# Kernel tuning notes

Measured on AMD Instinct MI355X. Metric: run time of the kernel, lower is better.

Reference implementation:

```python
import jax, jax.numpy as jnp
import numpy as np

B, C, T = 16, 2048, 128      # batch, enc_in (variables), d_model
ID, NC, CD, GD, OUT = 32, 16, 32, 32, 96  # id_dim, num_clusters, cluster_dim, graph_dim, out_len
GIN = T + ID + CD            # gcn_input_dim = 192
NEG = -1.0e9


def setup_inputs() -> dict:
    key = jax.random.key(0)
    ks = jax.random.split(key, 13)
    s = 0.02
    return {
        "x": jax.random.normal(ks[0], (B, C, 1, T), dtype=jnp.float32),
        "id_emb": jax.random.normal(ks[1], (C, ID), dtype=jnp.float32) * s,
        "w1": jax.random.normal(ks[2], (T, T // 2), dtype=jnp.float32) * s,
        "b1": jnp.zeros((T // 2,), dtype=jnp.float32),
        "w2": jax.random.normal(ks[3], (T // 2, ID), dtype=jnp.float32) * s,
        "b2": jnp.zeros((ID,), dtype=jnp.float32),
        "cluster_emb": jax.random.normal(ks[4], (NC, CD), dtype=jnp.float32) * s,
        "wic": jax.random.normal(ks[5], (ID, CD), dtype=jnp.float32) * s,
        "bic": jnp.zeros((CD,), dtype=jnp.float32),
        "wg": jax.random.normal(ks[6], (ID + CD, GD), dtype=jnp.float32) * s,
        "bg": jnp.zeros((GD,), dtype=jnp.float32),
        "context_weight": jax.random.normal(ks[7], (C, GIN), dtype=jnp.float32) * s,
        "wl": jax.random.normal(ks[8], (GIN, OUT), dtype=jnp.float32) * s,
        "bl": jnp.zeros((OUT,), dtype=jnp.float32),
    }


def reference(x, id_emb, w1, b1, w2, b2, cluster_emb, wic, bic, wg, bg,
              context_weight, wl, bl):
    b, c, n, t = x.shape
    xs = x[:, :, 0, :]                                       # [b,c,t] (squeeze dim -2)
    # dynamic id projection: Linear -> ReLU -> Linear
    dyn = jax.nn.relu(xs @ w1 + b1) @ w2 + b2                # [b,c,id]
    id_embeds = id_emb[None, :, :] + dyn                     # static + dynamic
    # soft cluster assignment
    id_for_clustering = id_embeds @ wic + bic                # [b,c,cd]
    probs = jax.nn.softmax(
        jnp.einsum('bcl,nl->bcn', id_for_clustering, cluster_emb), axis=-1)
    cluster_embeds = probs @ cluster_emb                     # [b,c,cd]
    # graph embedding and dynamic dense adjacency
    graph_emb = jnp.concatenate([id_embeds, cluster_embeds], axis=-1) @ wg + bg
    adj = jnp.einsum('bcg,bmg->bcm', graph_emb, graph_emb)   # [b,c,c]
    adj = jax.nn.relu(adj)
    neg = NEG * jnp.eye(c, dtype=adj.dtype)                  # [c,c], -1e9 on diag, 0 off-diag
    adj = adj + neg
    # torch.where(adj<=0, neg_inf_matrix, adj): off-diag nonpositive -> 0, diag -> -1e9
    adj = jnp.where(adj <= 0.0, neg, adj)
    adj = jax.nn.softmax(adj, axis=-1)
    # two-stage GCN aggregation (dropout is identity in eval mode)
    gcn_input = jnp.concatenate([xs, id_embeds, cluster_embeds], axis=-1)  # [b,c,GIN]
    agg = jnp.einsum('boi,bid->bod', adj, gcn_input)         # [b,c,GIN]
    w = jnp.tanh(jnp.einsum('bod,ol->bdl', agg, context_weight))  # [b,GIN,GIN]
    out = (jnp.einsum('bdl,bod->bol', w, gcn_input) + gcn_input) @ wl + bl  # [b,c,out_len]
    return out[:, :, None, :]                                # unsqueeze dim -2
```

## Files before the change

### kernel.cpp

```cpp
#include <hip/hip_runtime.h>
#include <hip/hip_bf16.h>


typedef __attribute__((ext_vector_type(8))) short short8;
typedef __attribute__((ext_vector_type(16))) float f32x16;

__device__ __forceinline__ unsigned short f2bf(float f) {
    __hip_bfloat16 h = __float2bfloat16(f);
    return *reinterpret_cast<unsigned short*>(&h);
}
__device__ __forceinline__ float bf2f(unsigned short u) {
    __hip_bfloat16 h = *reinterpret_cast<__hip_bfloat16*>(&u);
    return __bfloat162float(h);
}

__global__ __launch_bounds__(256) void k0_transpose_x(
    const float* __restrict__ x, unsigned short* __restrict__ vt)
{
    __shared__ float sT[64 * 133];
    const int t = threadIdx.x;
    const int m0 = blockIdx.x * 64;
    const int b = blockIdx.y;
    const float* xb = x + (size_t)b * 2048 * 128;
    #pragma unroll
    for (int kk = 0; kk < 8; ++kk) {
        int i = t + kk * 256;
        int mm = i >> 5, q4 = i & 31;
        float4 v = ((const float4*)(xb + (size_t)(m0 + mm) * 128))[q4];
        float* d = sT + mm * 133 + q4 * 4;
        d[0] = v.x; d[1] = v.y; d[2] = v.z; d[3] = v.w;
    }
    __syncthreads();
    const int mp = t & 31;
    const int ch0 = t >> 5;
    #pragma unroll
    for (int pass = 0; pass < 16; ++pass) {
        int ch = ch0 + pass * 8;
        unsigned int u0 = f2bf(sT[(2 * mp) * 133 + ch]);
        unsigned int u1 = f2bf(sT[(2 * mp + 1) * 133 + ch]);
        *((unsigned int*)(vt + (size_t)(b * 192 + ch) * 2048 + m0) + mp) =
            u0 | (u1 << 16);
    }
}

__global__ __launch_bounds__(256) void k1_tiled(
    const float* __restrict__ x, const float* __restrict__ id_emb,
    const float* __restrict__ w1, const float* __restrict__ b1,
    const float* __restrict__ w2, const float* __restrict__ b2,
    const float* __restrict__ ce, const float* __restrict__ wic,
    const float* __restrict__ bic, const float* __restrict__ wg,
    const float* __restrict__ bg, unsigned short* __restrict__ vt,
    unsigned short* __restrict__ geb16)
{
    __shared__ float sh[32 * 68];
    __shared__ float sid[32 * 36];
    __shared__ float sic[32 * 36];
    __shared__ float scl[32 * 36];
    __shared__ float sp[32 * 20];

    const int t = threadIdx.x;
    const int r0 = blockIdx.x * 32;
    const int b = r0 >> 11;
    const int c0 = r0 & 2047;

    {
        const int row = t >> 3, j0 = (t & 7) * 8;
        const float* xrow = x + (size_t)(r0 + row) * 128;
        float acc[8];
        #pragma unroll
        for (int j = 0; j < 8; ++j) acc[j] = b1[j0 + j];
        float4 pa[4], pb[4];
        float4 pxv;
        #pragma unroll
        for (int u = 0; u < 4; ++u) {
            const float4* wr = (const float4*)(w1 + u * 64 + j0);
            pa[u] = wr[0]; pb[u] = wr[1];
        }
        pxv = *(const float4*)(xrow);
        for (int k0 = 0; k0 < 128; k0 += 4) {
            float4 ca[4], cb[4];
            float4 cxv = pxv;
            #pragma unroll
            for (int u = 0; u < 4; ++u) { ca[u] = pa[u]; cb[u] = pb[u]; }
            const int kn = k0 + 4;
            if (kn < 128) {
                #pragma unroll
                for (int u = 0; u < 4; ++u) {
                    const float4* wr = (const float4*)(w1 + (kn + u) * 64 + j0);
                    pa[u] = wr[0]; pb[u] = wr[1];
                }
                pxv = *(const float4*)(xrow + kn);
            }
            float cx[4] = {cxv.x, cxv.y, cxv.z, cxv.w};
            #pragma unroll
            for (int u = 0; u < 4; ++u) {
                acc[0] = fmaf(cx[u], ca[u].x, acc[0]);
                acc[1] = fmaf(cx[u], ca[u].y, acc[1]);
                acc[2] = fmaf(cx[u], ca[u].z, acc[2]);
                acc[3] = fmaf(cx[u], ca[u].w, acc[3]);
                acc[4] = fmaf(cx[u], cb[u].x, acc[4]);
                acc[5] = fmaf(cx[u], cb[u].y, acc[5]);
                acc[6] = fmaf(cx[u], cb[u].z, acc[6]);
                acc[7] = fmaf(cx[u], cb[u].w, acc[7]);
            }
        }
        float* hr = sh + row * 68 + j0;
        #pragma unroll
        for (int j = 0; j < 8; ++j) hr[j] = fmaxf(acc[j], 0.f);
    }
    __syncthreads();

    {
        const int row = t >> 3, j0 = (t & 7) * 4;
        const int c = c0 + row;
        const float* hrow = sh + row * 68;
        float acc[4];
        #pragma unroll
        for (int j = 0; j < 4; ++j) acc[j] = b2[j0 + j];
        float4 pw[4];
        float  ph[4];
        #pragma unroll
        for (int u = 0; u < 4; ++u) {
            pw[u] = *(const float4*)(w2 + u * 32 + j0);
            ph[u] = hrow[u];
        }
        for (int k0 = 0; k0 < 64; k0 += 4) {
            float4 cw4[4];
            float  ch4[4];
            #pragma unroll
            for (int u = 0; u < 4; ++u) { cw4[u] = pw[u]; ch4[u] = ph[u]; }
            const int kn = k0 + 4;
            if (kn < 64) {
                #pragma unroll
                for (int u = 0; u < 4; ++u) {
                    pw[u] = *(const float4*)(w2 + (kn + u) * 32 + j0);
                    ph[u] = hrow[kn + u];
                }
            }
            #pragma unroll
            for (int u = 0; u < 4; ++u) {
                acc[0] = fmaf(ch4[u], cw4[u].x, acc[0]);
                acc[1] = fmaf(ch4[u], cw4[u].y, acc[1]);
                acc[2] = fmaf(ch4[u], cw4[u].z, acc[2]);
                acc[3] = fmaf(ch4[u], cw4[u].w, acc[3]);
            }
        }
        #pragma unroll
        for (int j = 0; j < 4; ++j) {
            float ide = id_emb[c * 32 + j0 + j] + acc[j];
            sid[row * 36 + j0 + j] = ide;
            vt[(size_t)(b * 192 + 128 + j0 + j) * 2048 + c] = f2bf(ide);
        }
    }
    __syncthreads();

    {
        const int row = t >> 3, j0 = (t & 7) * 4;
        const float* irow = sid + row * 36;
        float acc[4];
        #pragma unroll
        for (int j = 0; j < 4; ++j) acc[j] = bic[j0 + j];
        float4 pw[4];
        float  pi[4];
        #pragma unroll
        for (int u = 0; u < 4; ++u) {
            pw[u] = *(const float4*)(wic + u * 32 + j0);
            pi[u] = irow[u];
        }
        for (int k0 = 0; k0 < 32; k0 += 4) {
            float4 cw4[4];
            float  ci4[4];
            #pragma unroll
            for (int u = 0; u < 4; ++u) { cw4[u] = pw[u]; ci4[u] = pi[u]; }
            const int kn = k0 + 4;
            if (kn < 32) {
                #pragma unroll
                for (int u = 0; u < 4; ++u) {
                    pw[u] = *(const float4*)(wic + (kn + u) * 32 + j0);
                    pi[u] = irow[kn + u];
                }
            }
            #pragma unroll
            for (int u = 0; u < 4; ++u) {
                acc[0] = fmaf(ci4[u], cw4[u].x, acc[0]);
                acc[1] = fmaf(ci4[u], cw4[u].y, acc[1]);
                acc[2] = fmaf(ci4[u], cw4[u].z, acc[2]);
                acc[3] = fmaf(ci4[u], cw4[u].w, acc[3]);
            }
        }
        #pragma unroll
        for (int j = 0; j < 4; ++j) sic[row * 36 + j0 + j] = acc[j];
    }
    __syncthreads();

    {
        const int n = t & 15, rowp = t >> 4;
        const float* cer = ce + n * 32;
        float a0 = 0.f, a1 = 0.f;
        #pragma unroll
        for (int k0 = 0; k0 < 32; k0 += 8) {
            float cv[8], s0[8], s1[8];
            #pragma unroll
            for (int u = 0; u < 8; ++u) {
                cv[u] = cer[k0 + u];
                s0[u] = sic[rowp * 36 + k0 + u];
                s1[u] = sic[(rowp + 16) * 36 + k0 + u];
            }
            #pragma unroll
            for (int u = 0; u < 8; ++u) {
                a0 = fmaf(s0[u], cv[u], a0);
                a1 = fmaf(s1[u], cv[u], a1);
            }
        }
        sp[rowp * 20 + n] = a0;
        sp[(rowp + 16) * 20 + n] = a1;
    }
    __syncthreads();

    if (t < 32) {
        float* pr = sp + t * 20;
        float mx = pr[0];
        for (int n = 1; n < 16; ++n) mx = fmaxf(mx, pr[n]);
        float ss = 0.f;
        for (int n = 0; n < 16; ++n) { float e = __expf(pr[n] - mx); pr[n] = e; ss += e; }
        float inv = 1.f / ss;
        for (int n = 0; n < 16; ++n) pr[n] *= inv;
    }
    __syncthreads();

    {
        const int row = t >> 3, j0 = (t & 7) * 4;
        const int c = c0 + row;
        const float* prow = sp + row * 20;
        float acc[4] = {0.f, 0.f, 0.f, 0.f};
        float4 pc[4];
        float  pp[4];
        #pragma unroll
        for (int u = 0; u < 4; ++u) {
            pc[u] = *(const float4*)(ce + u * 32 + j0);
            pp[u] = prow[u];
        }
        for (int n0 = 0; n0 < 16; n0 += 4) {
            float4 cc4[4];
            float  cp4[4];
            #pragma unroll
            for (int u = 0; u < 4; ++u) { cc4[u] = pc[u]; cp4[u] = pp[u]; }
            const int nn = n0 + 4;
            if (nn < 16) {
                #pragma unroll
                for (int u = 0; u < 4; ++u) {
                    pc[u] = *(const float4*)(ce + (nn + u) * 32 + j0);
                    pp[u] = prow[nn + u];
                }
            }
            #pragma unroll
            for (int u = 0; u < 4; ++u) {
                acc[0] = fmaf(cp4[u], cc4[u].x, acc[0]);
                acc[1] = fmaf(cp4[u], cc4[u].y, acc[1]);
                acc[2] = fmaf(cp4[u], cc4[u].z, acc[2]);
                acc[3] = fmaf(cp4[u], cc4[u].w, acc[3]);
            }
        }
        #pragma unroll
        for (int j = 0; j < 4; ++j) {
            scl[row * 36 + j0 + j] = acc[j];
            vt[(size_t)(b * 192 + 160 + j0 + j) * 2048 + c] = f2bf(acc[j]);
        }
    }
    __syncthreads();

    {
        const int row = t >> 3, j0 = (t & 7) * 4;
        const int r = r0 + row;
        const float* irow = sid + row * 36;
        const float* crow = scl + row * 36;
        float acc[4];
        #pragma unroll
        for (int j = 0; j < 4; ++j) acc[j] = bg[j0 + j];
        {
            float4 pw[4];
            float  pi[4];
            #pragma unroll
            for (int u = 0; u < 4; ++u) {
                pw[u] = *(const float4*)(wg + u * 32 + j0);
                pi[u] = irow[u];
            }
            for (int k0 = 0; k0 < 32; k0 += 4) {
                float4 cw4[4];
                float  ci4[4];
                #pragma unroll
                for (int u = 0; u < 4; ++u) { cw4[u] = pw[u]; ci4[u] = pi[u]; }
                const int kn = k0 + 4;
                if (kn < 32) {
                    #pragma unroll
                    for (int u = 0; u < 4; ++u) {
                        pw[u] = *(const float4*)(wg + (kn + u) * 32 + j0);
                        pi[u] = irow[kn + u];
                    }
                }
                #pragma unroll
                for (int u = 0; u < 4; ++u) {
                    acc[0] = fmaf(ci4[u], cw4[u].x, acc[0]);
                    acc[1] = fmaf(ci4[u], cw4[u].y, acc[1]);
                    acc[2] = fmaf(ci4[u], cw4[u].z, acc[2]);
                    acc[3] = fmaf(ci4[u], cw4[u].w, acc[3]);
                }
            }
        }
        {
            float4 pw[4];
            float  pcv[4];
            #pragma unroll
            for (int u = 0; u < 4; ++u) {
                pw[u] = *(const float4*)(wg + (32 + u) * 32 + j0);
                pcv[u] = crow[u];
            }
            for (int k0 = 0; k0 < 32; k0 += 4) {
                float4 cw4[4];
                float  cc4[4];
                #pragma unroll
                for (int u = 0; u < 4; ++u) { cw4[u] = pw[u]; cc4[u] = pcv[u]; }
                const int kn = k0 + 4;
                if (kn < 32) {
                    #pragma unroll
                    for (int u = 0; u < 4; ++u) {
                        pw[u] = *(const float4*)(wg + (32 + kn + u) * 32 + j0);
                        pcv[u] = crow[kn + u];
                    }
                }
                #pragma unroll
                for (int u = 0; u < 4; ++u) {
                    acc[0] = fmaf(cc4[u], cw4[u].x, acc[0]);
                    acc[1] = fmaf(cc4[u], cw4[u].y, acc[1]);
                    acc[2] = fmaf(cc4[u], cw4[u].z, acc[2]);
                    acc[3] = fmaf(cc4[u], cw4[u].w, acc[3]);
                }
            }
        }
        #pragma unroll
        for (int j = 0; j < 4; ++j)
            geb16[(size_t)r * 32 + j0 + j] = f2bf(acc[j]);
    }
}

__global__ __launch_bounds__(256) void k1b_sumv(
    const unsigned short* __restrict__ vt, float* __restrict__ sumv)
{
    __shared__ float red[256];
    const int ch = blockIdx.x, b = blockIdx.y, t = threadIdx.x;
    const unsigned short* row = vt + (size_t)(b * 192 + ch) * 2048;
    float a = 0.f;
    #pragma unroll
    for (int j = 0; j < 8; ++j) a += bf2f(row[t * 8 + j]);
    red[t] = a; __syncthreads();
    for (int off = 128; off > 0; off >>= 1) {
        if (t < off) red[t] += red[t + off];
        __syncthreads();
    }
    if (t == 0) sumv[b * 192 + ch] = red[0];
}

__global__ __launch_bounds__(256) void k2_fused(
    const unsigned short* __restrict__ geb16,
    const unsigned short* __restrict__ vt,
    const float* __restrict__ sumv,
    unsigned short* __restrict__ aggb)
{
    __shared__ unsigned short sGeO[64 * 40];
    __shared__ unsigned short sGe[2][64 * 40];
    __shared__ unsigned short sVtA[2][192 * 72];
    __shared__ unsigned short dw[64 * 72];
    __shared__ float s_sum[192];
    __shared__ float sinv[64];
    float* lpbuf = (float*)sVtA;

    const int t = threadIdx.x;
    const int lin = blockIdx.x + gridDim.x * blockIdx.y;
    const int nb = (lin & 7) * 64 + (lin >> 3);
    const int o0 = (nb & 31) * 64;
    const int b = nb >> 5;
    const unsigned short* geb = geb16 + (size_t)b * 2048 * 32;
    const unsigned short* vtb = vt + (size_t)b * 192 * 2048;

    const int lane = t & 63;
    const int mg = t >> 6;
    const int col = lane & 31;
    const int grp = lane >> 5;
    const int os = (mg & 1) * 32;
    const int ms = (mg >> 1) * 32;
    const int orow0 = (mg & 1) * 32;
    const int dbase = (mg >> 1) * 96;

    const int ge_row = t >> 2, ge_c8 = t & 3;

    short8 rGe;
    short8 rVt0, rVt1, rVt2, rVt3, rVt4, rVt5;

    if (t < 192) s_sum[t] = sumv[b * 192 + t];
    {
        short8 v = *(const short8*)(geb + (size_t)(o0 + ge_row) * 32 + ge_c8 * 8);
        *(short8*)(sGeO + ge_row * 40 + ge_c8 * 8) = v;
    }
    {
        rGe = *(const short8*)(geb + (size_t)ge_row * 32 + ge_c8 * 8);
        int i0;
        i0 = t + 0 * 256; rVt0 = *(const short8*)(vtb + (size_t)(i0 >> 3) * 2048 + 0 + (i0 & 7) * 8);
        i0 = t + 1 * 256; rVt1 = *(const short8*)(vtb + (size_t)(i0 >> 3) * 2048 + 0 + (i0 & 7) * 8);
        i0 = t + 2 * 256; rVt2 = *(const short8*)(vtb + (size_t)(i0 >> 3) * 2048 + 0 + (i0 & 7) * 8);
        i0 = t + 3 * 256; rVt3 = *(const short8*)(vtb + (size_t)(i0 >> 3) * 2048 + 0 + (i0 & 7) * 8);
        i0 = t + 4 * 256; rVt4 = *(const short8*)(vtb + (size_t)(i0 >> 3) * 2048 + 0 + (i0 & 7) * 8);
        i0 = t + 5 * 256; rVt5 = *(const short8*)(vtb + (size_t)(i0 >> 3) * 2048 + 0 + (i0 & 7) * 8);
    }
    {
        *(short8*)(sGe[0] + ge_row * 40 + ge_c8 * 8) = rGe;
        int i0;
        i0 = t + 0 * 256; *(short8*)(sVtA[0] + (i0 >> 3) * 72 + (i0 & 7) * 8) = rVt0;
        i0 = t + 1 * 256; *(short8*)(sVtA[0] + (i0 >> 3) * 72 + (i0 & 7) * 8) = rVt1;
        i0 = t + 2 * 256; *(short8*)(sVtA[0] + (i0 >> 3) * 72 + (i0 & 7) * 8) = rVt2;
        i0 = t + 3 * 256; *(short8*)(sVtA[0] + (i0 >> 3) * 72 + (i0 & 7) * 8) = rVt3;
        i0 = t + 4 * 256; *(short8*)(sVtA[0] + (i0 >> 3) * 72 + (i0 & 7) * 8) = rVt4;
        i0 = t + 5 * 256; *(short8*)(sVtA[0] + (i0 >> 3) * 72 + (i0 & 7) * 8) = rVt5;
    }
    __syncthreads();

    f32x16 acc0, acc1, acc2;
    #pragma unroll
    for (int i = 0; i < 16; ++i) { acc0[i] = 0.f; acc1[i] = 0.f; acc2[i] = 0.f; }
    float lpA[16];
    #pragma unroll
    for (int i = 0; i < 16; ++i) lpA[i] = 0.f;

    int cur = 0;
    for (int m0 = 0; m0 < 2048; m0 += 64) {
        const bool have_next = (m0 + 64 < 2048);

        if (have_next) {
            const int mn = m0 + 64;
            rGe = *(const short8*)(geb + (size_t)(mn + ge_row) * 32 + ge_c8 * 8);
            int i0;
            i0 = t + 0 * 256; rVt0 = *(const short8*)(vtb + (size_t)(i0 >> 3) * 2048 + mn + (i0 & 7) * 8);
            i0 = t + 1 * 256; rVt1 = *(const short8*)(vtb + (size_t)(i0 >> 3) * 2048 + mn + (i0 & 7) * 8);
            i0 = t + 2 * 256; rVt2 = *(const short8*)(vtb + (size_t)(i0 >> 3) * 2048 + mn + (i0 & 7) * 8);
            i0 = t + 3 * 256; rVt3 = *(const short8*)(vtb + (size_t)(i0 >> 3) * 2048 + mn + (i0 & 7) * 8);
            i0 = t + 4 * 256; rVt4 = *(const short8*)(vtb + (size_t)(i0 >> 3) * 2048 + mn + (i0 & 7) * 8);
            i0 = t + 5 * 256; rVt5 = *(const short8*)(vtb + (size_t)(i0 >> 3) * 2048 + mn + (i0 & 7) * 8);
        }

        f32x16 sacc;
        #pragma unroll
        for (int i = 0; i < 16; ++i) sacc[i] = 0.f;
        #pragma unroll
        for (int ks = 0; ks < 2; ++ks) {
            short8 A  = *(const short8*)(sGeO + (os + col) * 40 + ks * 16 + grp * 8);
            short8 Bf = *(const short8*)(sGe[cur] + (ms + col) * 40 + ks * 16 + grp * 8);
            sacc = __builtin_amdgcn_mfma_f32_32x32x16_bf16(A, Bf, sacc, 0, 0, 0);
        }
        {
            const int m_local = ms + col;
            if (m0 != o0) {
                #pragma unroll
                for (int r = 0; r < 16; ++r) {
                    int o_local = os + (r & 3) + 8 * (r >> 2) + 4 * grp;
                    float s = sacc[r];
                    float d = (s > 0.f) ? (__expf(s) - 1.f) : 0.f;
                    lpA[r] += d;
                    dw[o_local * 72 + m_local] = f2bf(d);
                }
            } else {
                const int gm = m0 + m_local;
                #pragma unroll
                for (int r = 0; r < 16; ++r) {
                    int o_local = os + (r & 3) + 8 * (r >> 2) + 4 * grp;
                    float s = sacc[r];
                    float d = (gm == o0 + o_local) ? -1.f
                            : ((s > 0.f) ? (__expf(s) - 1.f) : 0.f);
                    lpA[r] += d;
                    dw[o_local * 72 + m_local] = f2bf(d);
                }
            }
        }
        __syncthreads();

        #pragma unroll
        for (int ks = 0; ks < 4; ++ks) {
            short8 A  = *(const short8*)(dw + (orow0 + col) * 72 + ks * 16 + grp * 8);
            short8 B0 = *(const short8*)(sVtA[cur] + (dbase + col) * 72 + ks * 16 + grp * 8);
            short8 B1 = *(const short8*)(sVtA[cur] + (dbase + 32 + col) * 72 + ks * 16 + grp * 8);
            short8 B2 = *(const short8*)(sVtA[cur] + (dbase + 64 + col) * 72 + ks * 16 + grp * 8);
            acc0 = __builtin_amdgcn_mfma_f32_32x32x16_bf16(A, B0, acc0, 0, 0, 0);
            acc1 = __builtin_amdgcn_mfma_f32_32x32x16_bf16(A, B1, acc1, 0, 0, 0);
            acc2 = __builtin_amdgcn_mfma_f32_32x32x16_bf16(A, B2, acc2, 0, 0, 0);
        }

        if (have_next) {
            const int nbuf = cur ^ 1;
            *(short8*)(sGe[nbuf] + ge_row * 40 + ge_c8 * 8) = rGe;
            int i0;
            i0 = t + 0 * 256; *(short8*)(sVtA[nbuf] + (i0 >> 3) * 72 + (i0 & 7) * 8) = rVt0;
            i0 = t + 1 * 256; *(short8*)(sVtA[nbuf] + (i0 >> 3) * 72 + (i0 & 7) * 8) = rVt1;
            i0 = t + 2 * 256; *(short8*)(sVtA[nbuf] + (i0 >> 3) * 72 + (i0 & 7) * 8) = rVt2;
            i0 = t + 3 * 256; *(short8*)(sVtA[nbuf] + (i0 >> 3) * 72 + (i0 & 7) * 8) = rVt3;
            i0 = t + 4 * 256; *(short8*)(sVtA[nbuf] + (i0 >> 3) * 72 + (i0 & 7) * 8) = rVt4;
            i0 = t + 5 * 256; *(short8*)(sVtA[nbuf] + (i0 >> 3) * 72 + (i0 & 7) * 8) = rVt5;
        }
        __syncthreads();
        cur ^= 1;
    }

    {
        const int widx = mg >> 1;
        #pragma unroll
        for (int r = 0; r < 16; ++r) {
            int ol = os + (r & 3) + 8 * (r >> 2) + 4 * grp;
            lpbuf[(widx * 32 + col) * 68 + ol] = lpA[r];
        }
    }
    __syncthreads();
    if (t < 64) {
        float l = 2048.f;
        for (int i = 0; i < 64; ++i) l += lpbuf[i * 68 + t];
        sinv[t] = 1.f / l;
    }
    __syncthreads();

    {
        f32x16 av[3] = {acc0, acc1, acc2};
        unsigned short* ab = aggb + (size_t)b * 2048 * 192;
        #pragma unroll
        for (int n = 0; n < 3; ++n) {
            int chn = dbase + n * 32 + col;
            float sv = s_sum[chn];
            #pragma unroll
            for (int r = 0; r < 16; ++r) {
                int ol = orow0 + (r & 3) + 8 * (r >> 2) + 4 * grp;
                ab[(size_t)(o0 + ol) * 192 + chn] =
                    f2bf((sv + av[n][r]) * sinv[ol]);
            }
        }
    }
}

__global__ __launch_bounds__(256) void k3_ctx_sk(
    const unsigned short* __restrict__ aggb, const float* __restrict__ cw,
    float* __restrict__ wpart)
{
    __shared__ float sA[64 * 68];
    __shared__ float sW[64 * 68];
    const int t = threadIdx.x;
    const int slot = blockIdx.z;
    const int b = slot >> 3;
    const int ks = slot & 7;
    const int d0 = blockIdx.x * 64;
    const int l0 = blockIdx.y * 64;
    const unsigned short* ab = aggb + (size_t)b * 2048 * 192;
    const int ti = t >> 4, tj = t & 15;
    float acc[4][4] = {{0.f}};

    for (int o0 = ks * 256; o0 < ks * 256 + 256; o0 += 64) {
        for (int i = t; i < 4096; i += 256) {
            int oo = i >> 6, dd = i & 63;
            sA[oo * 68 + dd] = bf2f(ab[(size_t)(o0 + oo) * 192 + d0 + dd]);
            sW[oo * 68 + dd] = cw[(size_t)(o0 + oo) * 192 + l0 + dd];
        }
        __syncthreads();
        for (int o = 0; o < 64; ++o) {
            const float* ap = sA + o * 68 + ti * 4;
            const float* wp = sW + o * 68 + tj * 4;
            float a0 = ap[0], a1 = ap[1], a2 = ap[2], a3 = ap[3];
            float w0 = wp[0], w1v = wp[1], w2v = wp[2], w3 = wp[3];
            acc[0][0] = fmaf(a0, w0, acc[0][0]); acc[0][1] = fmaf(a0, w1v, acc[0][1]);
            acc[0][2] = fmaf(a0, w2v, acc[0][2]); acc[0][3] = fmaf(a0, w3, acc[0][3]);
            acc[1][0] = fmaf(a1, w0, acc[1][0]); acc[1][1] = fmaf(a1, w1v, acc[1][1]);
            acc[1][2] = fmaf(a1, w2v, acc[1][2]); acc[1][3] = fmaf(a1, w3, acc[1][3]);
            acc[2][0] = fmaf(a2, w0, acc[2][0]); acc[2][1] = fmaf(a2, w1v, acc[2][1]);
            acc[2][2] = fmaf(a2, w2v, acc[2][2]); acc[2][3] = fmaf(a2, w3, acc[2][3]);
            acc[3][0] = fmaf(a3, w0, acc[3][0]); acc[3][1] = fmaf(a3, w1v, acc[3][1]);
            acc[3][2] = fmaf(a3, w2v, acc[3][2]); acc[3][3] = fmaf(a3, w3, acc[3][3]);
        }
        __syncthreads();
    }
    float* wp = wpart + (size_t)slot * 36864;
    #pragma unroll
    for (int i = 0; i < 4; ++i)
        #pragma unroll
        for (int j = 0; j < 4; ++j)
            wp[(d0 + ti * 4 + i) * 192 + l0 + tj * 4 + j] = acc[i][j];
}

__global__ __launch_bounds__(256) void k3r_reduce(
    const float* __restrict__ wpart, float* __restrict__ wraw)
{
    const int idx = blockIdx.x * 256 + threadIdx.x;
    const int b = blockIdx.y;
    const float* base = wpart + (size_t)b * 8 * 36864 + idx;
    float a = 0.f;
    #pragma unroll
    for (int ks = 0; ks < 8; ++ks) a += base[(size_t)ks * 36864];
    wraw[(size_t)b * 36864 + idx] = tanhf(a);
}

__global__ __launch_bounds__(256) void k3_ctx(
    const unsigned short* __restrict__ aggb, const float* __restrict__ cw,
    float* __restrict__ wraw)
{
    __shared__ float sA[64 * 68];
    __shared__ float sW[64 * 68];
    const int t = threadIdx.x;
    const int b = blockIdx.z;
    const int d0 = blockIdx.x * 64;
    const int l0 = blockIdx.y * 64;
    const unsigned short* ab = aggb + (size_t)b * 2048 * 192;
    const int ti = t >> 4, tj = t & 15;
    float acc[4][4] = {{0.f}};

    for (int o0 = 0; o0 < 2048; o0 += 64) {
        for (int i = t; i < 4096; i += 256) {
            int oo = i >> 6, dd = i & 63;
            sA[oo * 68 + dd] = bf2f(ab[(size_t)(o0 + oo) * 192 + d0 + dd]);
            sW[oo * 68 + dd] = cw[(size_t)(o0 + oo) * 192 + l0 + dd];
        }
        __syncthreads();
        for (int o = 0; o < 64; ++o) {
            const float* ap = sA + o * 68 + ti * 4;
            const float* wp = sW + o * 68 + tj * 4;
            float a0 = ap[0], a1 = ap[1], a2 = ap[2], a3 = ap[3];
            float w0 = wp[0], w1v = wp[1], w2v = wp[2], w3 = wp[3];
            acc[0][0] = fmaf(a0, w0, acc[0][0]); acc[0][1] = fmaf(a0, w1v, acc[0][1]);
            acc[0][2] = fmaf(a0, w2v, acc[0][2]); acc[0][3] = fmaf(a0, w3, acc[0][3]);
            acc[1][0] = fmaf(a1, w0, acc[1][0]); acc[1][1] = fmaf(a1, w1v, acc[1][1]);
            acc[1][2] = fmaf(a1, w2v, acc[1][2]); acc[1][3] = fmaf(a1, w3, acc[1][3]);
            acc[2][0] = fmaf(a2, w0, acc[2][0]); acc[2][1] = fmaf(a2, w1v, acc[2][1]);
            acc[2][2] = fmaf(a2, w2v, acc[2][2]); acc[2][3] = fmaf(a2, w3, acc[2][3]);
            acc[3][0] = fmaf(a3, w0, acc[3][0]); acc[3][1] = fmaf(a3, w1v, acc[3][1]);
            acc[3][2] = fmaf(a3, w2v, acc[3][2]); acc[3][3] = fmaf(a3, w3, acc[3][3]);
        }
        __syncthreads();
    }
    float* wb = wraw + (size_t)b * 36864;
    #pragma unroll
    for (int i = 0; i < 4; ++i)
        #pragma unroll
        for (int j = 0; j < 4; ++j)
            wb[(d0 + ti * 4 + i) * 192 + l0 + tj * 4 + j] = tanhf(acc[i][j]);
}

__global__ __launch_bounds__(192) void k3b_m2(
    const float* __restrict__ wmat, const float* __restrict__ wl,
    float* __restrict__ m2)
{
    const int t = threadIdx.x;
    const int b = blockIdx.y;
    const int d = blockIdx.x * 2 + (t / 96);
    const int l = t % 96;
    const float* wrow = wmat + (size_t)b * 36864 + d * 192;
    float acc = wl[d * 96 + l];
    float pa[8], pb[8];
    #pragma unroll
    for (int u = 0; u < 8; ++u) { pa[u] = wrow[u]; pb[u] = wl[u * 96 + l]; }
    for (int k0 = 0; k0 < 192; k0 += 8) {
        float ca[8], cb[8];
        #pragma unroll
        for (int u = 0; u < 8; ++u) { ca[u] = pa[u]; cb[u] = pb[u]; }
        const int kn = k0 + 8;
        if (kn < 192) {
            #pragma unroll
            for (int u = 0; u < 8; ++u) {
                pa[u] = wrow[kn + u];
                pb[u] = wl[(kn + u) * 96 + l];
            }
        }
        #pragma unroll
        for (int u = 0; u < 8; ++u) acc = fmaf(ca[u], cb[u], acc);
    }
    m2[(size_t)b * 18432 + d * 96 + l] = acc;
}

__global__ __launch_bounds__(192) void k4_tiled(
    const float* __restrict__ x, const unsigned short* __restrict__ vt,
    const float* __restrict__ m2, const float* __restrict__ bl,
    float* __restrict__ out)
{
    __shared__ float sm2[192 * 96];
    const int t = threadIdx.x;
    const int rblk = blockIdx.x;
    const int b = blockIdx.y;
    {
        const float4* src = (const float4*)(m2 + (size_t)b * 18432);
        float4* dst = (float4*)sm2;
        #pragma unroll
        for (int i = 0; i < 24; ++i) dst[t + i * 192] = src[t + i * 192];
    }
    __syncthreads();

    const int rg = t / 12;
    const int cg = t % 12;
    const int j0 = cg * 8;
    const int cloc = rblk * 64 + rg * 4;
    const int rr = b * 2048 + cloc;
    float acc[4][8];
    #pragma unroll
    for (int i = 0; i < 4; ++i)
        #pragma unroll
        for (int j = 0; j < 8; ++j) acc[i][j] = bl[j0 + j];

    for (int k0 = 0; k0 < 128; k0 += 8) {
        float rv[4][8];
        #pragma unroll
        for (int i = 0; i < 4; ++i) {
            const float4* xr = (const float4*)(x + (size_t)(rr + i) * 128 + k0);
            float4 a = xr[0], c4 = xr[1];
            rv[i][0] = a.x; rv[i][1] = a.y; rv[i][2] = a.z; rv[i][3] = a.w;
            rv[i][4] = c4.x; rv[i][5] = c4.y; rv[i][6] = c4.z; rv[i][7] = c4.w;
        }
        #pragma unroll
        for (int kk = 0; kk < 8; ++kk) {
            const float* mr = sm2 + (k0 + kk) * 96 + j0;
            float mv[8];
            #pragma unroll
            for (int j = 0; j < 8; ++j) mv[j] = mr[j];
            #pragma unroll
            for (int i = 0; i < 4; ++i)
                #pragma unroll
                for (int j = 0; j < 8; ++j)
                    acc[i][j] = fmaf(rv[i][kk], mv[j], acc[i][j]);
        }
    }
    for (int k = 128; k < 192; ++k) {
        const unsigned short* vr = vt + (size_t)(b * 192 + k) * 2048 + cloc;
        float rv0 = bf2f(vr[0]), rv1 = bf2f(vr[1]);
        float rv2 = bf2f(vr[2]), rv3 = bf2f(vr[3]);
        const float* mr = sm2 + k * 96 + j0;
        #pragma unroll
        for (int j = 0; j < 8; ++j) {
            float mv = mr[j];
            acc[0][j] = fmaf(rv0, mv, acc[0][j]);
            acc[1][j] = fmaf(rv1, mv, acc[1][j]);
            acc[2][j] = fmaf(rv2, mv, acc[2][j]);
            acc[3][j] = fmaf(rv3, mv, acc[3][j]);
        }
    }
    #pragma unroll
    for (int i = 0; i < 4; ++i) {
        float* orow = out + (size_t)(rr + i) * 96 + j0;
        *(float4*)orow = make_float4(acc[i][0], acc[i][1], acc[i][2], acc[i][3]);
        *(float4*)(orow + 4) = make_float4(acc[i][4], acc[i][5], acc[i][6], acc[i][7]);
    }
}

extern "C" void kernel_launch(void* const* d_in, const int* in_sizes, int n_in,
                              void* d_out, int out_size, void* d_ws, size_t ws_size,
                              hipStream_t stream) {
    const float* x      = (const float*)d_in[0];
    const float* id_emb = (const float*)d_in[1];
    const float* w1     = (const float*)d_in[2];
    const float* b1     = (const float*)d_in[3];
    const float* w2     = (const float*)d_in[4];
    const float* b2     = (const float*)d_in[5];
    const float* ce     = (const float*)d_in[6];
    const float* wic    = (const float*)d_in[7];
    const float* bic    = (const float*)d_in[8];
    const float* wg     = (const float*)d_in[9];
    const float* bg     = (const float*)d_in[10];
    const float* cw     = (const float*)d_in[11];
    const float* wl     = (const float*)d_in[12];
    const float* bl     = (const float*)d_in[13];
    float* out = (float*)d_out;

    float* ws = (float*)d_ws;
    unsigned short* vt    = (unsigned short*)ws;
    unsigned short* geb16 = (unsigned short*)(ws + 3145728);
    unsigned short* aggb  = (unsigned short*)(ws + 3670016);
    float* wraw  = ws + 6815744;
    float* m2    = ws + 7405568;
    float* sumv  = ws + 7700480;
    float* wpart = ws + 7703552;
    const size_t need_sk = (7703552ull + 4718592ull) * 4ull;
    const bool use_sk = (ws_size >= need_sk);

    hipLaunchKernelGGL(k0_transpose_x, dim3(32, 16), dim3(256), 0, stream, x, vt);
    hipLaunchKernelGGL(k1_tiled, dim3(1024), dim3(256), 0, stream,
                       x, id_emb, w1, b1, w2, b2, ce, wic, bic, wg, bg, vt, geb16);
    hipLaunchKernelGGL(k1b_sumv, dim3(192, 16), dim3(256), 0, stream, vt, sumv);
    hipLaunchKernelGGL(k2_fused, dim3(32, 16), dim3(256), 0, stream,
                       geb16, vt, sumv, aggb);
    if (use_sk) {
        hipLaunchKernelGGL(k3_ctx_sk, dim3(3, 3, 128), dim3(256), 0, stream,
                           aggb, cw, wpart);
        hipLaunchKernelGGL(k3r_reduce, dim3(144, 16), dim3(256), 0, stream,
                           wpart, wraw);
    } else {
        hipLaunchKernelGGL(k3_ctx, dim3(3, 3, 16), dim3(256), 0, stream,
                           aggb, cw, wraw);
    }
    hipLaunchKernelGGL(k3b_m2, dim3(96, 16), dim3(192), 0, stream,
                       wraw, wl, m2);
    hipLaunchKernelGGL(k4_tiled, dim3(32, 16), dim3(192), 0, stream,
                       x, vt, m2, bl, out);
}
```

Measured before the change: 291.4 us.

## Compute context-weight contraction with bf16 MFMA using hi/lo split weights

Replaces the FP32 LDS-tiled split-K kernel for agg^T @ context_weight with a matrix-core version using 32x32x16 bf16 MFMA. The context weight is first split into bf16 high and low parts by a small pre-kernel, giving near-FP32 accuracy on the weight side. The aim is to take this stage off the scalar FP32 path. Operands are loaded straight from global memory with strided 2-byte reads and no LDS staging, which may be poorly coalesced. The kernel also needs extra workspace, and an additional launch converts the weights on every call.

```diff
diff --git a/kernel.cpp b/kernel.cpp
--- a/kernel.cpp
+++ b/kernel.cpp
@@ -537,6 +537,67 @@
                     f2bf((sv + av[n][r]) * sinv[ol]);
             }
         }
+    }
+}
+
+__global__ __launch_bounds__(256) void k3a_split(
+    const float* __restrict__ cw, unsigned short* __restrict__ cwhi,
+    unsigned short* __restrict__ cwlo)
+{
+    const int idx = blockIdx.x * 256 + threadIdx.x;
+    float v = cw[idx];
+    unsigned short h = f2bf(v);
+    cwhi[idx] = h;
+    cwlo[idx] = f2bf(v - bf2f(h));
+}
+
+__global__ __launch_bounds__(256) void k3_mfma_sk(
+    const unsigned short* __restrict__ aggb,
+    const unsigned short* __restrict__ cwhi,
+    const unsigned short* __restrict__ cwlo,
+    float* __restrict__ wpart)
+{
+    const int t = threadIdx.x;
+    const int slot = blockIdx.z;
+    const int b = slot >> 3;
+    const int ks = slot & 7;
+    const int d0 = blockIdx.x * 64;
+    const int l0 = blockIdx.y * 64;
+    const unsigned short* ab = aggb + (size_t)b * 2048 * 192;
+
+    const int lane = t & 63;
+    const int w = t >> 6;
+    const int col = lane & 31;
+    const int grp = lane >> 5;
+    const int drow = d0 + (w & 1) * 32 + col;
+    const int lrow = l0 + (w >> 1) * 32 + col;
+
+    f32x16 acc;
+    #pragma unroll
+    for (int i = 0; i < 16; ++i) acc[i] = 0.f;
+
+    const int obase = ks * 256;
+    #pragma unroll 4
+    for (int ostep = 0; ostep < 16; ++ostep) {
+        const int ob = obase + ostep * 16 + grp * 8;
+        short8 A, Bh, Bl;
+        #pragma unroll
+        for (int i = 0; i < 8; ++i) {
+            const size_t ro = (size_t)(ob + i) * 192;
+            A[i]  = (short)ab[ro + drow];
+            Bh[i] = (short)cwhi[ro + lrow];
+            Bl[i] = (short)cwlo[ro + lrow];
+        }
+        acc = __builtin_amdgcn_mfma_f32_32x32x16_bf16(A, Bh, acc, 0, 0, 0);
+        acc = __builtin_amdgcn_mfma_f32_32x32x16_bf16(A, Bl, acc, 0, 0, 0);
+    }
+
+    float* wp = wpart + (size_t)slot * 36864;
+    const int lcol = l0 + (w >> 1) * 32 + col;
+    #pragma unroll
+    for (int r = 0; r < 16; ++r) {
+        int dl = d0 + (w & 1) * 32 + (r & 3) + 8 * (r >> 2) + 4 * grp;
+        wp[(size_t)dl * 192 + lcol] = acc[r];
     }
 }
 
@@ -774,8 +835,12 @@
     float* m2    = ws + 7405568;
     float* sumv  = ws + 7700480;
     float* wpart = ws + 7703552;
-    const size_t need_sk = (7703552ull + 4718592ull) * 4ull;
-    const bool use_sk = (ws_size >= need_sk);
+    unsigned short* cwhi = (unsigned short*)(ws + 12422144);
+    unsigned short* cwlo = cwhi + 393216;
+    const size_t need_sk   = (7703552ull + 4718592ull) * 4ull;
+    const size_t need_mfma = (7703552ull + 4718592ull + 393216ull) * 4ull;
+    const bool use_mfma = (ws_size >= need_mfma);
+    const bool use_sk   = (ws_size >= need_sk);
 
     hipLaunchKernelGGL(k0_transpose_x, dim3(32, 16), dim3(256), 0, stream, x, vt);
     hipLaunchKernelGGL(k1_tiled, dim3(1024), dim3(256), 0, stream,
@@ -783,7 +848,14 @@
     hipLaunchKernelGGL(k1b_sumv, dim3(192, 16), dim3(256), 0, stream, vt, sumv);
     hipLaunchKernelGGL(k2_fused, dim3(32, 16), dim3(256), 0, stream,
                        geb16, vt, sumv, aggb);
-    if (use_sk) {
+    if (use_mfma) {
+        hipLaunchKernelGGL(k3a_split, dim3(1536), dim3(256), 0, stream,
+                           cw, cwhi, cwlo);
+        hipLaunchKernelGGL(k3_mfma_sk, dim3(3, 3, 128), dim3(256), 0, stream,
+                           aggb, cwhi, cwlo, wpart);
+        hipLaunchKernelGGL(k3r_reduce, dim3(144, 16), dim3(256), 0, stream,
+                           wpart, wraw);
+    } else if (use_sk) {
         hipLaunchKernelGGL(k3_ctx_sk, dim3(3, 3, 128), dim3(256), 0, stream,
                            aggb, cw, wpart);
         hipLaunchKernelGGL(k3r_reduce, dim3(144, 16), dim3(256), 0, stream,
```

Measured after the change: 273.3 us (median of 4 runs). -6.2%, faster.
